# Optimization experiments

Hardware: AMD Instinct MI355X
Metric: run time of the kernel (lower is better)

Reference implementation:

```python
import jax, jax.numpy as jnp
import numpy as np

B, S, H = 32, 2048, 1024

def setup_inputs() -> dict:
    key = jax.random.key(0)
    ks = jax.random.split(key, 8)
    scale = 1.0 / np.sqrt(H)
    return {
        "decoder_hidden": jax.random.normal(ks[0], (B, 1, H), dtype=jnp.float32),
        "encoder_outputs": jax.random.normal(ks[1], (B, S, H), dtype=jnp.float32),
        "coverage": jax.random.uniform(ks[2], (B, S), dtype=jnp.float32),
        "W_enc": jax.random.normal(ks[3], (H, H), dtype=jnp.float32) * scale,  # enc_v.weight [out,in]
        "W_dec": jax.random.normal(ks[4], (H, H), dtype=jnp.float32) * scale,  # dec_v.weight
        "b_dec": jax.random.normal(ks[5], (H,), dtype=jnp.float32) * scale,    # dec_v.bias
        "w_cov": jax.random.normal(ks[6], (H,), dtype=jnp.float32) * scale,    # cov_v.weight [H,1] squeezed
        "v": jax.random.normal(ks[7], (H,), dtype=jnp.float32) * scale,        # V_prime.weight [1,H] squeezed
    }

def reference(decoder_hidden, encoder_outputs, coverage, W_enc, W_dec, b_dec, w_cov, v):
    # enc_feature: [B,S,H]; torch Linear is x @ W.T
    enc_feature = jnp.einsum("bsh,oh->bso", encoder_outputs, W_enc)
    # dec_feature: [B,1,H], broadcasts over S
    dec_feature = jnp.einsum("bqh,oh->bqo", decoder_hidden, W_dec) + b_dec
    # cov_feature: coverage[...,None] @ w_cov[None,:] -> [B,S,H]
    cov_feature = coverage[..., None] * w_cov
    scores = jnp.tanh(enc_feature + dec_feature + cov_feature)  # [B,S,H]
    attn_scores = jnp.einsum("bsh,h->bs", scores, v)            # V_prime, squeeze(-1)
    attn_dist = jax.nn.softmax(attn_scores, axis=-1)[:, None, :]  # [B,1,S]
    return attn_dist
```

## Files before the change

### kernel.cpp

```cpp
#include <hip/hip_runtime.h>

#define Bb 32
#define Ss 2048
#define Hh 1024

typedef __attribute__((ext_vector_type(4))) float f32x4;
typedef __attribute__((ext_vector_type(8))) short s16x8;

#define GAS const __attribute__((address_space(1))) unsigned int
#define LAS __attribute__((address_space(3))) unsigned int

__device__ __forceinline__ unsigned short f2bf(float x) {
  unsigned int u = __float_as_uint(x);
  u = (u + 0x7fffu + ((u >> 16) & 1u)) >> 16;
  return (unsigned short)u;
}

__global__ void cvt_swz(const float* __restrict__ in, unsigned short* __restrict__ out) {
  int g = blockIdx.x * blockDim.x + threadIdx.x;
  int row = g >> 7, k8 = g & 127;
  const float4* src = reinterpret_cast<const float4*>(in + (size_t)row * Hh + k8 * 8);
  float4 a = src[0], b = src[1];
  union { unsigned short u[8]; uint4 q; } rr;
  rr.u[0] = f2bf(a.x); rr.u[1] = f2bf(a.y); rr.u[2] = f2bf(a.z); rr.u[3] = f2bf(a.w);
  rr.u[4] = f2bf(b.x); rr.u[5] = f2bf(b.y); rr.u[6] = f2bf(b.z); rr.u[7] = f2bf(b.w);
  int kt = k8 >> 3, kh = (k8 >> 2) & 1, k4 = k8 & 3;
  int r = row & 255;
  size_t byte = (size_t)(((row >> 8) * 16 + kt) * 2 + kh) * 16384
              + (size_t)(r * 64 + ((k4 ^ ((r >> 1) & 3)) << 4));
  *reinterpret_cast<uint4*>(reinterpret_cast<char*>(out) + byte) = rr.q;
}

__global__ void dec_feat_kernel(const float* __restrict__ dh,
                                const float* __restrict__ Wd,
                                const float* __restrict__ bd,
                                float* __restrict__ out) {
  int gw = blockIdx.x * 4 + (threadIdx.x >> 6);
  int lane = threadIdx.x & 63;
  int b = gw >> 10, o = gw & 1023;
  const float4* x = reinterpret_cast<const float4*>(dh + (size_t)b * Hh);
  const float4* w = reinterpret_cast<const float4*>(Wd + (size_t)o * Hh);
  float acc = 0.f;
#pragma unroll
  for (int it = 0; it < 4; ++it) {
    float4 xa = x[lane + it * 64];
    float4 wa = w[lane + it * 64];
    acc += xa.x * wa.x + xa.y * wa.y + xa.z * wa.z + xa.w * wa.w;
  }
#pragma unroll
  for (int m = 1; m < 64; m <<= 1) acc += __shfl_xor(acc, m, 64);
  if (lane == 0) out[gw] = acc + bd[o];
}

__global__ void __launch_bounds__(512, 2)
gemm8r(const unsigned short* __restrict__ Aw,
       const unsigned short* __restrict__ Bw,
       const float* __restrict__ decf,
       const float* __restrict__ cov,
       const float* __restrict__ wcov,
       const float* __restrict__ v,
       float* __restrict__ part) {
  __shared__ char lds[131072];

  const int bid = blockIdx.x;
  const int swz = (bid & 7) * 128 + (bid >> 3);
  const int s_tile = swz >> 2;
  const int ot = swz & 3;

  const int tid = threadIdx.x, lane = tid & 63, wid = tid >> 6;
  const int wm = wid >> 2, wn = wid & 3;
  const int fr = lane & 15, hi = lane >> 4;

  const char* gA = reinterpret_cast<const char*>(Aw) + (size_t)s_tile * 524288 + tid * 16;
  const char* gB = reinterpret_cast<const char*>(Bw) + (size_t)ot * 524288 + tid * 16;

  const int xslot = (hi ^ ((fr >> 1) & 3)) << 4;
  const int aRow = (wm * 128 + fr) * 64;
  const int bRow = 32768 + (wn * 64 + fr) * 64;

#define STAGE(jj) do {                                                            \
    int _j = (jj);                                                                \
    if (_j < 64) {                                                                \
      int _kt = _j >> 2, _h = _j & 3, _isB = _h & 1, _kh = _h >> 1;               \
      const char* _src = (_isB ? gB : gA) + (size_t)(_kt * 2 + _kh) * 16384;      \
      char* _dst = lds + (_kt & 1) * 65536 + _isB * 32768 + _kh * 16384 + tid * 16; \
      __builtin_amdgcn_global_load_lds((GAS*)(_src),        (LAS*)(_dst),        16, 0, 0); \
      __builtin_amdgcn_global_load_lds((GAS*)(_src + 8192), (LAS*)(_dst + 8192), 16, 0, 0); \
    }                                                                             \
  } while (0)

#define NW ((void)0)
#define VM6 asm volatile("s_waitcnt vmcnt(6)" ::: "memory")
#define VM4 asm volatile("s_waitcnt vmcnt(4)" ::: "memory")
#define VM0 asm volatile("s_waitcnt vmcnt(0)" ::: "memory")
#define KWAIT(t) do { if ((t) < 14) VM4; else if ((t) == 14) VM0; } while (0)

  f32x4 acc[8][4];
#pragma unroll
  for (int i = 0; i < 8; ++i)
#pragma unroll
    for (int j = 0; j < 4; ++j) acc[i][j] = (f32x4){0.f, 0.f, 0.f, 0.f};

  s16x8 bfr[4];

#define PH_B0(c, kh, jj, WAIT) do {                                               \
    const char* Lb = lds + (c) * 65536 + (kh) * 16384;                            \
    s16x8 afr[4];                                                                 \
    _Pragma("unroll") for (int fn = 0; fn < 4; ++fn)                              \
      bfr[fn] = *reinterpret_cast<const s16x8*>(Lb + bRow + fn * 1024 + xslot);   \
    _Pragma("unroll") for (int fm = 0; fm < 4; ++fm)                              \
      afr[fm] = *reinterpret_cast<const s16x8*>(Lb + aRow + fm * 1024 + xslot);   \
    STAGE(jj);                                                                    \
    __builtin_amdgcn_s_barrier();                                                 \
    asm volatile("s_waitcnt lgkmcnt(0)" ::: "memory");                            \
    __builtin_amdgcn_sched_barrier(0);                                            \
    __builtin_amdgcn_s_setprio(1);                                                \
    _Pragma("unroll") for (int fm = 0; fm < 4; ++fm)                              \
      _Pragma("unroll") for (int fn = 0; fn < 4; ++fn)                            \
        acc[fm][fn] = __builtin_amdgcn_mfma_f32_16x16x32_bf16(                    \
            afr[fm], bfr[fn], acc[fm][fn], 0, 0, 0);                              \
    __builtin_amdgcn_s_setprio(0);                                                \
    WAIT;                                                                         \
    __builtin_amdgcn_s_barrier();                                                 \
  } while (0)

#define PH_A1(c, kh, jj, WAIT) do {                                               \
    const char* Lb = lds + (c) * 65536 + (kh) * 16384;                            \
    s16x8 afr[4];                                                                 \
    _Pragma("unroll") for (int fm = 0; fm < 4; ++fm)                              \
      afr[fm] = *reinterpret_cast<const s16x8*>(Lb + aRow + 4096 + fm * 1024 + xslot); \
    STAGE(jj);                                                                    \
    __builtin_amdgcn_s_barrier();                                                 \
    asm volatile("s_waitcnt lgkmcnt(0)" ::: "memory");                            \
    __builtin_amdgcn_sched_barrier(0);                                            \
    __builtin_amdgcn_s_setprio(1);                                                \
    _Pragma("unroll") for (int fm = 0; fm < 4; ++fm)                              \
      _Pragma("unroll") for (int fn = 0; fn < 4; ++fn)                            \
        acc[4 + fm][fn] = __builtin_amdgcn_mfma_f32_16x16x32_bf16(                \
            afr[fm], bfr[fn], acc[4 + fm][fn], 0, 0, 0);                          \
    __builtin_amdgcn_s_setprio(0);                                                \
    WAIT;                                                                         \
    __builtin_amdgcn_s_barrier();                                                 \
  } while (0)

  STAGE(0); STAGE(1); STAGE(2); STAGE(3); STAGE(4); STAGE(5); STAGE(6);
  VM6;
  __builtin_amdgcn_s_barrier();

#pragma unroll 1
  for (int t = 0; t < 16; ++t) {
    const int c = t & 1;
    const int j0 = 4 * t + 7;
    PH_B0(c, 0, j0,     NW);
    PH_A1(c, 0, j0 + 1, NW);
    PH_B0(c, 1, j0 + 2, NW);
    PH_A1(c, 1, j0 + 3, KWAIT(t));
  }
#undef PH_B0
#undef PH_A1
#undef STAGE

  const int row0 = s_tile * 256 + wm * 128 + hi * 4;
  const int o0 = ot * 256 + wn * 64 + fr;
  const int bb = s_tile >> 3;

  float vv[4], wv[4], dv[4];
#pragma unroll
  for (int fn = 0; fn < 4; ++fn) {
    int o = o0 + fn * 16;
    vv[fn] = v[o];
    wv[fn] = wcov[o];
    dv[fn] = decf[bb * 1024 + o];
  }

  float* pout = part + (size_t)(ot * 4 + wn) * 65536;
#pragma unroll
  for (int i = 0; i < 8; ++i) {
#pragma unroll
    for (int r = 0; r < 4; ++r) {
      int s_flat = row0 + i * 16 + r;
      float cvv = cov[s_flat];
      float sum = 0.f;
#pragma unroll
      for (int fn = 0; fn < 4; ++fn) {
        float x = acc[i][fn][r] + dv[fn] + cvv * wv[fn];
        float xc = fminf(fmaxf(x, -15.f), 15.f);
        float e2 = __expf(2.f * xc);
        sum += (1.f - 2.f / (e2 + 1.f)) * vv[fn];
      }
      sum += __shfl_xor(sum, 1, 64);
      sum += __shfl_xor(sum, 2, 64);
      sum += __shfl_xor(sum, 4, 64);
      sum += __shfl_xor(sum, 8, 64);
      if (fr == 0) pout[s_flat] = sum;
    }
  }
}

__global__ void softmax_kernel(const float* __restrict__ part, float* __restrict__ out) {
  int b = blockIdx.x;
  int tid = threadIdx.x;
  int lane = tid & 63, w = tid >> 6;
  float vals[8];
#pragma unroll
  for (int k = 0; k < 8; ++k) {
    int idx = b * Ss + tid + k * 256;
    float s0 = 0.f;
#pragma unroll
    for (int j = 0; j < 16; ++j) s0 += part[j * 65536 + idx];
    vals[k] = s0;
  }
  float m = vals[0];
#pragma unroll
  for (int k = 1; k < 8; ++k) m = fmaxf(m, vals[k]);
#pragma unroll
  for (int off = 1; off < 64; off <<= 1) m = fmaxf(m, __shfl_xor(m, off, 64));
  __shared__ float sm[4], ss[4];
  if (lane == 0) sm[w] = m;
  __syncthreads();
  m = fmaxf(fmaxf(sm[0], sm[1]), fmaxf(sm[2], sm[3]));
  float s = 0.f;
#pragma unroll
  for (int k = 0; k < 8; ++k) { vals[k] = __expf(vals[k] - m); s += vals[k]; }
#pragma unroll
  for (int off = 1; off < 64; off <<= 1) s += __shfl_xor(s, off, 64);
  if (lane == 0) ss[w] = s;
  __syncthreads();
  s = ss[0] + ss[1] + ss[2] + ss[3];
  float inv = 1.f / s;
#pragma unroll
  for (int k = 0; k < 8; ++k) out[(size_t)b * Ss + tid + k * 256] = vals[k] * inv;
}

extern "C" void kernel_launch(void* const* d_in, const int* in_sizes, int n_in,
                              void* d_out, int out_size, void* d_ws, size_t ws_size,
                              hipStream_t stream) {
  const float* dh    = (const float*)d_in[0];
  const float* enc   = (const float*)d_in[1];
  const float* cov   = (const float*)d_in[2];
  const float* W_enc = (const float*)d_in[3];
  const float* W_dec = (const float*)d_in[4];
  const float* b_dec = (const float*)d_in[5];
  const float* w_cov = (const float*)d_in[6];
  const float* v     = (const float*)d_in[7];
  float* out = (float*)d_out;

  char* ws = (char*)d_ws;
  unsigned short* A_bf  = (unsigned short*)ws;
  unsigned short* W_bf  = (unsigned short*)(ws + 134217728);
  float*          decf  = (float*)(ws + 136314880);
  float*          part  = (float*)(ws + 136445952);

  cvt_swz<<<32768, 256, 0, stream>>>(enc, A_bf);
  cvt_swz<<<512, 256, 0, stream>>>(W_enc, W_bf);
  dec_feat_kernel<<<(Bb * Hh) / 4, 256, 0, stream>>>(dh, W_dec, b_dec, decf);
  gemm8r<<<1024, 512, 0, stream>>>(A_bf, W_bf, decf, cov, w_cov, v, part);
  softmax_kernel<<<Bb, 256, 0, stream>>>(part, out);
}
```

Measured before the change: 254.6 us.

## Restructure GEMM main loop into two phases per K-tile with wider staging

Replaces the four-phase-per-iteration schedule (each phase covering half a K-tile) with two phases per iteration that each cover the full 64-wide K-tile. All of A for the next tile is staged in the first phase and B for two tiles ahead in the second. This halves the number of barrier pairs per K-tile and gives each phase twice as many MFMAs to hide LDS reads and global loads behind. The cost is more fragment registers live at once and a changed prefetch distance, which could raise register pressure or expose load latency.

```diff
diff --git a/kernel.cpp b/kernel.cpp
--- a/kernel.cpp
+++ b/kernel.cpp
@@ -53,7 +53,7 @@
 }
 
 __global__ void __launch_bounds__(512, 2)
-gemm8r(const unsigned short* __restrict__ Aw,
+gemm2p(const unsigned short* __restrict__ Aw,
        const unsigned short* __restrict__ Bw,
        const float* __restrict__ decf,
        const float* __restrict__ cov,
@@ -76,24 +76,27 @@
 
   const int xslot = (hi ^ ((fr >> 1) & 3)) << 4;
   const int aRow = (wm * 128 + fr) * 64;
-  const int bRow = 32768 + (wn * 64 + fr) * 64;
-
-#define STAGE(jj) do {                                                            \
-    int _j = (jj);                                                                \
-    if (_j < 64) {                                                                \
-      int _kt = _j >> 2, _h = _j & 3, _isB = _h & 1, _kh = _h >> 1;               \
-      const char* _src = (_isB ? gB : gA) + (size_t)(_kt * 2 + _kh) * 16384;      \
-      char* _dst = lds + (_kt & 1) * 65536 + _isB * 32768 + _kh * 16384 + tid * 16; \
-      __builtin_amdgcn_global_load_lds((GAS*)(_src),        (LAS*)(_dst),        16, 0, 0); \
-      __builtin_amdgcn_global_load_lds((GAS*)(_src + 8192), (LAS*)(_dst + 8192), 16, 0, 0); \
-    }                                                                             \
+  const int bRow = (wn * 64 + fr) * 64;
+
+#define STAGE_A2(tt) do {                                                         \
+    const char* _s = gA + (size_t)(tt) * 32768;                                   \
+    char* _d = lds + ((tt) & 1) * 65536 + tid * 16;                               \
+    __builtin_amdgcn_global_load_lds((GAS*)(_s),         (LAS*)(_d),         16, 0, 0); \
+    __builtin_amdgcn_global_load_lds((GAS*)(_s + 8192),  (LAS*)(_d + 8192),  16, 0, 0); \
+    __builtin_amdgcn_global_load_lds((GAS*)(_s + 16384), (LAS*)(_d + 16384), 16, 0, 0); \
+    __builtin_amdgcn_global_load_lds((GAS*)(_s + 24576), (LAS*)(_d + 24576), 16, 0, 0); \
   } while (0)
-
-#define NW ((void)0)
-#define VM6 asm volatile("s_waitcnt vmcnt(6)" ::: "memory")
+#define STAGE_B2(tt) do {                                                         \
+    const char* _s = gB + (size_t)(tt) * 32768;                                   \
+    char* _d = lds + ((tt) & 1) * 65536 + 32768 + tid * 16;                       \
+    __builtin_amdgcn_global_load_lds((GAS*)(_s),         (LAS*)(_d),         16, 0, 0); \
+    __builtin_amdgcn_global_load_lds((GAS*)(_s + 8192),  (LAS*)(_d + 8192),  16, 0, 0); \
+    __builtin_amdgcn_global_load_lds((GAS*)(_s + 16384), (LAS*)(_d + 16384), 16, 0, 0); \
+    __builtin_amdgcn_global_load_lds((GAS*)(_s + 24576), (LAS*)(_d + 24576), 16, 0, 0); \
+  } while (0)
+
 #define VM4 asm volatile("s_waitcnt vmcnt(4)" ::: "memory")
 #define VM0 asm volatile("s_waitcnt vmcnt(0)" ::: "memory")
-#define KWAIT(t) do { if ((t) < 14) VM4; else if ((t) == 14) VM0; } while (0)
 
   f32x4 acc[8][4];
 #pragma unroll
@@ -101,64 +104,78 @@
 #pragma unroll
     for (int j = 0; j < 4; ++j) acc[i][j] = (f32x4){0.f, 0.f, 0.f, 0.f};
 
-  s16x8 bfr[4];
-
-#define PH_B0(c, kh, jj, WAIT) do {                                               \
-    const char* Lb = lds + (c) * 65536 + (kh) * 16384;                            \
-    s16x8 afr[4];                                                                 \
-    _Pragma("unroll") for (int fn = 0; fn < 4; ++fn)                              \
-      bfr[fn] = *reinterpret_cast<const s16x8*>(Lb + bRow + fn * 1024 + xslot);   \
-    _Pragma("unroll") for (int fm = 0; fm < 4; ++fm)                              \
-      afr[fm] = *reinterpret_cast<const s16x8*>(Lb + aRow + fm * 1024 + xslot);   \
-    STAGE(jj);                                                                    \
-    __builtin_amdgcn_s_barrier();                                                 \
-    asm volatile("s_waitcnt lgkmcnt(0)" ::: "memory");                            \
-    __builtin_amdgcn_sched_barrier(0);                                            \
-    __builtin_amdgcn_s_setprio(1);                                                \
-    _Pragma("unroll") for (int fm = 0; fm < 4; ++fm)                              \
-      _Pragma("unroll") for (int fn = 0; fn < 4; ++fn)                            \
-        acc[fm][fn] = __builtin_amdgcn_mfma_f32_16x16x32_bf16(                    \
-            afr[fm], bfr[fn], acc[fm][fn], 0, 0, 0);                              \
-    __builtin_amdgcn_s_setprio(0);                                                \
-    WAIT;                                                                         \
-    __builtin_amdgcn_s_barrier();                                                 \
-  } while (0)
-
-#define PH_A1(c, kh, jj, WAIT) do {                                               \
-    const char* Lb = lds + (c) * 65536 + (kh) * 16384;                            \
-    s16x8 afr[4];                                                                 \
-    _Pragma("unroll") for (int fm = 0; fm < 4; ++fm)                              \
-      afr[fm] = *reinterpret_cast<const s16x8*>(Lb + aRow + 4096 + fm * 1024 + xslot); \
-    STAGE(jj);                                                                    \
-    __builtin_amdgcn_s_barrier();                                                 \
-    asm volatile("s_waitcnt lgkmcnt(0)" ::: "memory");                            \
-    __builtin_amdgcn_sched_barrier(0);                                            \
-    __builtin_amdgcn_s_setprio(1);                                                \
-    _Pragma("unroll") for (int fm = 0; fm < 4; ++fm)                              \
-      _Pragma("unroll") for (int fn = 0; fn < 4; ++fn)                            \
-        acc[4 + fm][fn] = __builtin_amdgcn_mfma_f32_16x16x32_bf16(                \
-            afr[fm], bfr[fn], acc[4 + fm][fn], 0, 0, 0);                          \
-    __builtin_amdgcn_s_setprio(0);                                                \
-    WAIT;                                                                         \
-    __builtin_amdgcn_s_barrier();                                                 \
-  } while (0)
-
-  STAGE(0); STAGE(1); STAGE(2); STAGE(3); STAGE(4); STAGE(5); STAGE(6);
-  VM6;
+  s16x8 bfr[2][4];
+
+  STAGE_A2(0); STAGE_B2(0); STAGE_B2(1);
+  VM4;
   __builtin_amdgcn_s_barrier();
 
 #pragma unroll 1
   for (int t = 0; t < 16; ++t) {
     const int c = t & 1;
-    const int j0 = 4 * t + 7;
-    PH_B0(c, 0, j0,     NW);
-    PH_A1(c, 0, j0 + 1, NW);
-    PH_B0(c, 1, j0 + 2, NW);
-    PH_A1(c, 1, j0 + 3, KWAIT(t));
-  }
-#undef PH_B0
-#undef PH_A1
-#undef STAGE
+    const char* LA0 = lds + c * 65536;
+    const char* LA1 = LA0 + 16384;
+    const char* LB0 = LA0 + 32768;
+    const char* LB1 = LA0 + 49152;
+
+    {
+      s16x8 af0[4], af1[4];
+#pragma unroll
+      for (int fn = 0; fn < 4; ++fn) {
+        bfr[0][fn] = *reinterpret_cast<const s16x8*>(LB0 + bRow + fn * 1024 + xslot);
+        bfr[1][fn] = *reinterpret_cast<const s16x8*>(LB1 + bRow + fn * 1024 + xslot);
+      }
+#pragma unroll
+      for (int fm = 0; fm < 4; ++fm) {
+        af0[fm] = *reinterpret_cast<const s16x8*>(LA0 + aRow + fm * 1024 + xslot);
+        af1[fm] = *reinterpret_cast<const s16x8*>(LA1 + aRow + fm * 1024 + xslot);
+      }
+      if (t < 15) STAGE_A2(t + 1);
+      __builtin_amdgcn_s_barrier();
+      asm volatile("s_waitcnt lgkmcnt(0)" ::: "memory");
+      __builtin_amdgcn_sched_barrier(0);
+      __builtin_amdgcn_s_setprio(1);
+#pragma unroll
+      for (int fm = 0; fm < 4; ++fm)
+#pragma unroll
+        for (int fn = 0; fn < 4; ++fn) {
+          acc[fm][fn] = __builtin_amdgcn_mfma_f32_16x16x32_bf16(
+              af0[fm], bfr[0][fn], acc[fm][fn], 0, 0, 0);
+          acc[fm][fn] = __builtin_amdgcn_mfma_f32_16x16x32_bf16(
+              af1[fm], bfr[1][fn], acc[fm][fn], 0, 0, 0);
+        }
+      __builtin_amdgcn_s_setprio(0);
+      __builtin_amdgcn_s_barrier();
+    }
+
+    {
+      s16x8 af0[4], af1[4];
+#pragma unroll
+      for (int fm = 0; fm < 4; ++fm) {
+        af0[fm] = *reinterpret_cast<const s16x8*>(LA0 + aRow + 4096 + fm * 1024 + xslot);
+        af1[fm] = *reinterpret_cast<const s16x8*>(LA1 + aRow + 4096 + fm * 1024 + xslot);
+      }
+      if (t < 14) STAGE_B2(t + 2);
+      __builtin_amdgcn_s_barrier();
+      asm volatile("s_waitcnt lgkmcnt(0)" ::: "memory");
+      __builtin_amdgcn_sched_barrier(0);
+      __builtin_amdgcn_s_setprio(1);
+#pragma unroll
+      for (int fm = 0; fm < 4; ++fm)
+#pragma unroll
+        for (int fn = 0; fn < 4; ++fn) {
+          acc[4 + fm][fn] = __builtin_amdgcn_mfma_f32_16x16x32_bf16(
+              af0[fm], bfr[0][fn], acc[4 + fm][fn], 0, 0, 0);
+          acc[4 + fm][fn] = __builtin_amdgcn_mfma_f32_16x16x32_bf16(
+              af1[fm], bfr[1][fn], acc[4 + fm][fn], 0, 0, 0);
+        }
+      __builtin_amdgcn_s_setprio(0);
+      if (t < 14) { VM4; } else if (t == 14) { VM0; }
+      __builtin_amdgcn_s_barrier();
+    }
+  }
+#undef STAGE_A2
+#undef STAGE_B2
 
   const int row0 = s_tile * 256 + wm * 128 + hi * 4;
   const int o0 = ot * 256 + wn * 64 + fr;
@@ -254,6 +271,6 @@
   cvt_swz<<<32768, 256, 0, stream>>>(enc, A_bf);
   cvt_swz<<<512, 256, 0, stream>>>(W_enc, W_bf);
   dec_feat_kernel<<<(Bb * Hh) / 4, 256, 0, stream>>>(dh, W_dec, b_dec, decf);
-  gemm8r<<<1024, 512, 0, stream>>>(A_bf, W_bf, decf, cov, w_cov, v, part);
+  gemm2p<<<1024, 512, 0, stream>>>(A_bf, W_bf, decf, cov, w_cov, v, part);
   softmax_kernel<<<Bb, 256, 0, stream>>>(part, out);
 }
```

New measurement: 252.6 us. No clear change (-0.8%).
